# Performance work log

Measured on AMD Instinct MI355X. Metric: run time of the kernel, lower is better.

Reference implementation:

```python
import jax, jax.numpy as jnp
import numpy as np

D_MODEL = 1024
N_HEADS = 16
DFF = 4096
B, S = 2, 2048
EPS = 1e-6


def _dense_params(key, d_in, d_out):
    kw, kb = jax.random.split(key)
    w = jax.random.normal(kw, (d_in, d_out), jnp.float32) * 0.02
    b = jax.random.normal(kb, (d_out,), jnp.float32) * 0.02
    return w, b


def setup_inputs() -> dict:
    key = jax.random.key(0)
    ks = jax.random.split(key, 20)
    inp = {
        "x": jax.random.normal(ks[0], (B, S, D_MODEL), jnp.float32),
        "enc_output": jax.random.normal(ks[1], (B, S, D_MODEL), jnp.float32),
        # causal look-ahead mask: 1 where attention is NOT allowed
        "look_ahead_mask": jnp.triu(jnp.ones((S, S), jnp.float32), k=1)[None, None],
        "padding_mask": (jax.random.uniform(ks[2], (B, 1, 1, S)) < 0.1).astype(jnp.float32),
    }
    names = ["mha1_wq", "mha1_wk", "mha1_wv", "mha1_wo",
             "mha2_wq", "mha2_wk", "mha2_wv", "mha2_wo"]
    for i, n in enumerate(names):
        w, b = _dense_params(ks[3 + i], D_MODEL, D_MODEL)
        inp[n] = w
        inp[n.replace("w", "b")] = b
    inp["ffn_w1"], inp["ffn_b1"] = _dense_params(ks[11], D_MODEL, DFF)
    inp["ffn_w2"], inp["ffn_b2"] = _dense_params(ks[12], DFF, D_MODEL)
    for i, n in enumerate(["ln1", "ln2", "ln3"]):
        inp[n + "_g"] = jnp.ones((D_MODEL,), jnp.float32)
        inp[n + "_b"] = jnp.zeros((D_MODEL,), jnp.float32)
    return inp


def _layernorm(x, g, b):
    mu = jnp.mean(x, axis=-1, keepdims=True)
    var = jnp.mean(jnp.square(x - mu), axis=-1, keepdims=True)
    return (x - mu) * jax.lax.rsqrt(var + EPS) * g + b


def _mha(v, k, q, mask, wq, bq, wk, bk, wv, bv, wo, bo):
    Bq, Sq, D = q.shape
    depth = D // N_HEADS

    def split(t):  # [B,S,D] -> [B,H,S,depth]
        return t.reshape(t.shape[0], -1, N_HEADS, depth).transpose(0, 2, 1, 3)

    qh = split(q @ wq + bq)
    kh = split(k @ wk + bk)
    vh = split(v @ wv + bv)
    logits = jnp.einsum("bhqd,bhkd->bhqk", qh, kh) / jnp.sqrt(jnp.float32(depth))
    if mask is not None:
        logits = logits + mask * (-1e9)
    attn = jax.nn.softmax(logits, axis=-1)
    out = jnp.einsum("bhqk,bhkd->bhqd", attn, vh)
    out = out.transpose(0, 2, 1, 3).reshape(Bq, Sq, D)
    return out @ wo + bo


def reference(x, enc_output, look_ahead_mask, padding_mask,
              mha1_wq, mha1_bq, mha1_wk, mha1_bk, mha1_wv, mha1_bv, mha1_wo, mha1_bo,
              mha2_wq, mha2_bq, mha2_wk, mha2_bk, mha2_wv, mha2_bv, mha2_wo, mha2_bo,
              ffn_w1, ffn_b1, ffn_w2, ffn_b2,
              ln1_g, ln1_b, ln2_g, ln2_b, ln3_g, ln3_b):
    # self-attention (training=False -> dropout is identity)
    attn1 = _mha(x, x, x, look_ahead_mask,
                 mha1_wq, mha1_bq, mha1_wk, mha1_bk, mha1_wv, mha1_bv, mha1_wo, mha1_bo)
    out1 = _layernorm(x + attn1, ln1_g, ln1_b)
    # cross-attention: q from decoder, k/v from encoder output
    attn2 = _mha(enc_output, enc_output, out1, padding_mask,
                 mha2_wq, mha2_bq, mha2_wk, mha2_bk, mha2_wv, mha2_bv, mha2_wo, mha2_bo)
    out2 = _layernorm(out1 + attn2, ln2_g, ln2_b)
    ffn = jax.nn.relu(out2 @ ffn_w1 + ffn_b1) @ ffn_w2 + ffn_b2
    return _layernorm(out2 + ffn, ln3_g, ln3_b)
```

## Files before the change

kernel.cpp:

```cpp
#include <hip/hip_runtime.h>
#include <hip/hip_bf16.h>
#include <stdint.h>

#define DM   1024
#define NH   16
#define SS   2048
#define BB   2
#define MT   4096

typedef __attribute__((ext_vector_type(8))) short short8;
typedef __attribute__((ext_vector_type(4))) float f32x4;

typedef __attribute__((address_space(1))) const unsigned int as1_uint;
typedef __attribute__((address_space(3))) unsigned int as3_uint;

__device__ __forceinline__ void async16(const void* g, void* l) {
  __builtin_amdgcn_global_load_lds((as1_uint*)g, (as3_uint*)l, 16, 0, 0);
}

#define WAITV(n) asm volatile("s_waitcnt vmcnt(" #n ")" ::: "memory")
#define BARRIER_SB() do { __builtin_amdgcn_s_barrier(); __builtin_amdgcn_sched_barrier(0); } while (0)
#define EXP2(x) __builtin_amdgcn_exp2f(x)

__device__ __forceinline__ unsigned short f2bf(float f) {
  union { float f; unsigned u; } c; c.f = f;
  unsigned r = c.u + 0x7fffu + ((c.u >> 16) & 1u);
  return (unsigned short)(r >> 16);
}

__device__ __forceinline__ unsigned cvt_pk_bf16(float lo, float hi) {
  unsigned r;
  asm("v_cvt_pk_bf16_f32 %0, %1, %2" : "=v"(r) : "v"(lo), "v"(hi));
  return r;
}

__device__ __forceinline__ float swz16(float x) {
  return __uint_as_float((unsigned)__builtin_amdgcn_ds_swizzle((int)__float_as_uint(x), 0x401F));
}

__device__ __forceinline__ void xcd_swz(int& bx, int& by, int& bz) {
  int GX = gridDim.x, GY = gridDim.y;
  int nwg = GX * GY * gridDim.z;
  int old = blockIdx.x + GX * (blockIdx.y + GY * blockIdx.z);
  int f2 = (old & 7) * (nwg >> 3) + (old >> 3);
  bz = f2 / (GX * GY);
  int rem = f2 % (GX * GY);
  bx = rem / GY;
  by = rem % GY;
}

__global__ __launch_bounds__(256) void k_conv2(
    const float* __restrict__ a, const float* __restrict__ b,
    unsigned short* __restrict__ oa, unsigned short* __restrict__ ob) {
  int bxr = blockIdx.x;
  const float* in = (bxr < 4096) ? a : b;
  unsigned short* out = (bxr < 4096) ? oa : ob;
  int i = ((bxr & 4095) * 256 + threadIdx.x) * 4;
  float4 v = *(const float4*)(in + i);
  uint2 u;
  u.x = (unsigned)f2bf(v.x) | ((unsigned)f2bf(v.y) << 16);
  u.y = (unsigned)f2bf(v.z) | ((unsigned)f2bf(v.w) << 16);
  *(uint2*)(out + i) = u;
}

__global__ __launch_bounds__(256) void k_transpose_bf16(
    const float* __restrict__ in, unsigned short* __restrict__ out, int R, int C) {
  __shared__ float t[64][65];
  int c0 = blockIdx.x * 64, r0 = blockIdx.y * 64;
  int tx = threadIdx.x & 63, ty = threadIdx.x >> 6;
#pragma unroll
  for (int i = 0; i < 16; i++)
    t[ty + i * 4][tx] = in[(size_t)(r0 + ty + i * 4) * C + c0 + tx];
  __syncthreads();
#pragma unroll
  for (int i = 0; i < 16; i++)
    out[(size_t)(c0 + ty + i * 4) * R + r0 + tx] = f2bf(t[tx][ty + i * 4]);
}

struct PtrArr { const float* p[8]; };
__global__ __launch_bounds__(256) void k_transpose8(
    PtrArr ps, unsigned short* __restrict__ out0) {
  __shared__ float t[64][65];
  const float* in = ps.p[blockIdx.z];
  unsigned short* out = out0 + (size_t)blockIdx.z * 1048576;
  int c0 = blockIdx.x * 64, r0 = blockIdx.y * 64;
  int tx = threadIdx.x & 63, ty = threadIdx.x >> 6;
#pragma unroll
  for (int i = 0; i < 16; i++)
    t[ty + i * 4][tx] = in[(size_t)(r0 + ty + i * 4) * 1024 + c0 + tx];
  __syncthreads();
#pragma unroll
  for (int i = 0; i < 16; i++)
    out[(size_t)(c0 + ty + i * 4) * 1024 + r0 + tx] = f2bf(t[tx][ty + i * 4]);
}

template<int BM, int OUT_MODE, bool RELU, bool RESID, bool SPLITK>
__global__ __launch_bounds__(256) void k_gemm(
    const unsigned short* __restrict__ A,
    const unsigned short* __restrict__ Bt,
    const float* __restrict__ bias,
    const float* __restrict__ resid,
    void* __restrict__ outp, void* __restrict__ outp2,
    int M, int N, int K, int KS) {
  __shared__ unsigned short Alds[3][BM * 32];
  __shared__ unsigned short Blds[3][128 * 32];
  int tid = threadIdx.x;
  int w = tid >> 6, lane = tid & 63;
  int l15 = lane & 15, l4 = lane >> 4;
  int bxs, bys, bzs;
  xcd_swz(bxs, bys, bzs);
  int brow = bys * BM, bcol = bxs * 128;

  constexpr int MR = 4;
  constexpr int NR = (BM == 128) ? 4 : 2;
  int wr = (BM == 128) ? (w >> 1) : 0;
  int wc = (BM == 128) ? (w & 1) : w;
  int rbase = wr * 64;
  int cbase = wc * (NR * 16);

  f32x4 acc[MR][NR];
#pragma unroll
  for (int i = 0; i < MR; i++)
#pragma unroll
    for (int j = 0; j < NR; j++) acc[i][j] = (f32x4){0.f, 0.f, 0.f, 0.f};

#define STAGEG(bufi, kk) do {                                                  \
    _Pragma("unroll")                                                          \
    for (int c = 0; c < BM / 64; c++) {                                        \
      int elem = (c * 256 + tid) * 8;                                          \
      int row = elem >> 5, col = elem & 31;                                    \
      async16(A + (size_t)(brow + row) * K + (kk) + col, &Alds[bufi][elem]);   \
    }                                                                          \
    _Pragma("unroll")                                                          \
    for (int c = 0; c < 2; c++) {                                              \
      int elem = (c * 256 + tid) * 8;                                          \
      int row = elem >> 5, col = elem & 31;                                    \
      async16(Bt + (size_t)(bcol + row) * K + (kk) + col, &Blds[bufi][elem]);  \
    } } while (0)

  int kbeg = SPLITK ? bzs * KS : 0;
  int nk = KS / 32;
  STAGEG(0, kbeg);
  if (nk > 1) {
    STAGEG(1, kbeg + 32);
    if (BM == 128) WAITV(4); else WAITV(3);
  } else {
    WAITV(0);
  }
  BARRIER_SB();

  for (int t = 0; t < nk; t++) {
    int buf = t % 3;
    if (t + 2 < nk) STAGEG((t + 2) % 3, kbeg + (t + 2) * 32);
    short8 af[MR], bfr[NR];
#pragma unroll
    for (int i = 0; i < MR; i++)
      af[i] = *(const short8*)&Alds[buf][(rbase + i * 16 + l15) * 32 + l4 * 8];
#pragma unroll
    for (int j = 0; j < NR; j++)
      bfr[j] = *(const short8*)&Blds[buf][(cbase + j * 16 + l15) * 32 + l4 * 8];
#pragma unroll
    for (int i = 0; i < MR; i++)
#pragma unroll
      for (int j = 0; j < NR; j++)
        acc[i][j] = __builtin_amdgcn_mfma_f32_16x16x32_bf16(af[i], bfr[j], acc[i][j], 0, 0, 0);
    if (t + 2 < nk) {
      if (BM == 128) WAITV(4); else WAITV(3);
    } else if (t + 1 < nk) {
      WAITV(0);
    }
    if (t + 1 < nk) BARRIER_SB();
  }
#undef STAGEG

  void* op = (SPLITK && bzs) ? outp2 : outp;
#pragma unroll
  for (int i = 0; i < MR; i++)
#pragma unroll
    for (int j = 0; j < NR; j++) {
      int row = brow + rbase + i * 16 + l4 * 4;
      int col = bcol + cbase + j * 16 + l15;
      float bs = (SPLITK || !bias) ? 0.f : bias[col];
#pragma unroll
      for (int r = 0; r < 4; r++) {
        float v = acc[i][j][r] + bs;
        if (RESID) v += resid[(size_t)(row + r) * N + col];
        if (RELU) v = fmaxf(v, 0.f);
        if (OUT_MODE == 0) ((float*)op)[(size_t)(row + r) * N + col] = v;
        else               ((unsigned short*)op)[(size_t)(row + r) * N + col] = f2bf(v);
      }
    }
}

__global__ __launch_bounds__(256) void k_gemm_qkv(
    const unsigned short* __restrict__ a0, const unsigned short* __restrict__ a1,
    const unsigned short* __restrict__ a2,
    const unsigned short* __restrict__ Bt,
    const float* __restrict__ b0, const float* __restrict__ b1, const float* __restrict__ b2,
    unsigned short* __restrict__ o0, unsigned short* __restrict__ o1, unsigned short* __restrict__ o2,
    int vmat, int M, int K) {
  __shared__ unsigned short Alds[3][128 * 32];
  __shared__ unsigned short Blds[3][128 * 32];
  int tid = threadIdx.x;
  int w = tid >> 6, lane = tid & 63;
  int wr = w >> 1, wc = w & 1;
  int l15 = lane & 15, l4 = lane >> 4;
  int bxs, bys, z;
  xcd_swz(bxs, bys, z);
  const unsigned short* A  = (z == 0) ? a0 : (z == 1) ? a1 : a2;
  const unsigned short* Bz = Bt + (size_t)z * 1048576;
  int brow = bys * 128, bcol = bxs * 128;

  f32x4 acc[4][4];
#pragma unroll
  for (int i = 0; i < 4; i++)
#pragma unroll
    for (int j = 0; j < 4; j++) acc[i][j] = (f32x4){0.f, 0.f, 0.f, 0.f};

#define STAGEQ(bufi, kk) do {                                                  \
    _Pragma("unroll")                                                          \
    for (int c = 0; c < 2; c++) {                                              \
      int elem = (c * 256 + tid) * 8;                                          \
      int row = elem >> 5, col = elem & 31;                                    \
      async16(A + (size_t)(brow + row) * K + (kk) + col, &Alds[bufi][elem]);   \
      async16(Bz + (size_t)(bcol + row) * K + (kk) + col, &Blds[bufi][elem]);  \
    } } while (0)

  int nk = K / 32;
  STAGEQ(0, 0);
  STAGEQ(1, 32);
  WAITV(4);
  BARRIER_SB();

  for (int t = 0; t < nk; t++) {
    int buf = t % 3;
    if (t + 2 < nk) STAGEQ((t + 2) % 3, (t + 2) * 32);
    short8 af[4], bfr[4];
#pragma unroll
    for (int i = 0; i < 4; i++) {
      af[i]  = *(const short8*)&Alds[buf][(wr * 64 + i * 16 + l15) * 32 + l4 * 8];
      bfr[i] = *(const short8*)&Blds[buf][(wc * 64 + i * 16 + l15) * 32 + l4 * 8];
    }
#pragma unroll
    for (int i = 0; i < 4; i++)
#pragma unroll
      for (int j = 0; j < 4; j++)
        acc[i][j] = __builtin_amdgcn_mfma_f32_16x16x32_bf16(af[i], bfr[j], acc[i][j], 0, 0, 0);
    if (t + 2 < nk) WAITV(4);
    else if (t + 1 < nk) WAITV(0);
    if (t + 1 < nk) BARRIER_SB();
  }
#undef STAGEQ

  const float* bias = (z == 0) ? b0 : (z == 1) ? b1 : b2;
  unsigned short* op = (z == 0) ? o0 : (z == 1) ? o1 : o2;
  bool tr = (z == vmat);
#pragma unroll
  for (int i = 0; i < 4; i++)
#pragma unroll
    for (int j = 0; j < 4; j++) {
      int row = brow + wr * 64 + i * 16 + l4 * 4;
      int colL = bcol + wc * 64 + j * 16 + l15;
      float bs = bias[colL];
#pragma unroll
      for (int r = 0; r < 4; r++) {
        float v = acc[i][j][r] + bs;
        if (tr) op[(size_t)colL * M + row + r] = f2bf(v);
        else    op[(size_t)(row + r) * 1024 + colL] = f2bf(v);
      }
    }
}

template<bool CAUSAL, int NF>
__global__ __launch_bounds__(256) void k_attn(
    const unsigned short* __restrict__ Q,
    const unsigned short* __restrict__ Kb,
    const unsigned short* __restrict__ Vt,
    const float* __restrict__ pm,
    unsigned short* __restrict__ out) {
  __shared__ unsigned short Klds[3][64 * 64];
  __shared__ unsigned short Vlds[3][64 * 64];
  __shared__ unsigned short Pw[4][NF][16 * 72];
  int tid = threadIdx.x, w = tid >> 6, lane = tid & 63;
  int l15 = lane & 15, l4 = lane >> 4;
  int h = blockIdx.y, b = blockIdx.z;
  const float SC = 0.125f * 1.44269504089f;
  const int NPASS = CAUSAL ? 2 : 1;

#define STAGE(bufi, kt_) do {                                                  \
    _Pragma("unroll")                                                          \
    for (int c = 0; c < 2; c++) {                                              \
      int e0 = w * 1024 + c * 512;                                             \
      int elem = e0 + lane * 8;                                                \
      int row_ = elem >> 6;                                                    \
      int col_ = (elem & 63) ^ ((row_ & 7) << 3);                              \
      async16(Kb + (size_t)(b * SS + (kt_) * 64 + row_) * DM + h * 64 + col_,  \
              &Klds[bufi][elem]);                                              \
      async16(Vt + (size_t)(h * 64 + row_) * MT + b * SS + (kt_) * 64 + col_,  \
              &Vlds[bufi][elem]);                                              \
    } } while (0)

  for (int pass = 0; pass < NPASS; pass++) {
    int qt = CAUSAL ? (pass == 0 ? (31 - (int)blockIdx.x) : (int)blockIdx.x)
                    : (int)blockIdx.x;
    int qbase = qt * (NF * 64) + w * (NF * 16);

    short8 qf[NF][2];
#pragma unroll
    for (int f = 0; f < NF; f++) {
      size_t qrow = (size_t)b * SS + qbase + f * 16 + l15;
#pragma unroll
      for (int ks = 0; ks < 2; ks++)
        qf[f][ks] = *(const short8*)(Q + qrow * DM + h * 64 + ks * 32 + l4 * 8);
    }

    float mrow[NF], lrow[NF];
    f32x4 accO[NF][4];
#pragma unroll
    for (int f = 0; f < NF; f++) {
      mrow[f] = -1e30f; lrow[f] = 0.f;
#pragma unroll
      for (int d = 0; d < 4; d++) accO[f][d] = (f32x4){0.f, 0.f, 0.f, 0.f};
    }

    int ktend = CAUSAL ? qt : (SS / 64 - 1);
    if (pass) BARRIER_SB();
    STAGE(0, 0);
    if (ktend >= 1) { STAGE(1, 1); WAITV(4); } else { WAITV(0); }
    BARRIER_SB();

    for (int kt = 0; kt <= ktend; kt++) {
      int buf = kt % 3;
      if (kt + 2 <= ktend) STAGE((kt + 2) % 3, kt + 2);

      bool active = !CAUSAL || (kt * 64 <= qbase + NF * 16 - 1);
      if (active) {
        f32x4 sa[NF][4];
#pragma unroll
        for (int f = 0; f < NF; f++)
#pragma unroll
          for (int nt = 0; nt < 4; nt++) sa[f][nt] = (f32x4){0.f, 0.f, 0.f, 0.f};
        __builtin_amdgcn_s_setprio(1);
#pragma unroll
        for (int ks = 0; ks < 2; ks++)
#pragma unroll
          for (int nt = 0; nt < 4; nt++) {
            int kr = nt * 16 + l15;
            short8 kf = *(const short8*)&Klds[buf][kr * 64 + ((ks * 32 + l4 * 8) ^ ((kr & 7) << 3))];
#pragma unroll
            for (int f = 0; f < NF; f++)
              sa[f][nt] = __builtin_amdgcn_mfma_f32_16x16x32_bf16(kf, qf[f][ks], sa[f][nt], 0, 0, 0);
          }
        __builtin_amdgcn_s_setprio(0);

        float pmb[16];
        if (!CAUSAL) {
#pragma unroll
          for (int nt = 0; nt < 4; nt++) {
            float4 pmv = *(const float4*)(pm + b * SS + kt * 64 + nt * 16 + l4 * 4);
#pragma unroll
            for (int r = 0; r < 4; r++) pmb[nt * 4 + r] = ((const float*)&pmv)[r] * -1e30f;
          }
        }
        bool diag = CAUSAL && (kt * 64 + 63 > qbase);

        float sv[NF][16], tm[NF];
#pragma unroll
        for (int f = 0; f < NF; f++) {
          if (CAUSAL && !diag) {
#pragma unroll
            for (int i = 0; i < 16; i++) sv[f][i] = sa[f][i >> 2][i & 3] * SC;
          } else if (CAUSAL) {
#pragma unroll
            for (int nt = 0; nt < 4; nt++)
#pragma unroll
              for (int r = 0; r < 4; r++) {
                float s = sa[f][nt][r] * SC;
                int kg = kt * 64 + nt * 16 + l4 * 4 + r;
                int qg = qbase + f * 16 + l15;
                if (kg > qg) s = -1e30f;
                sv[f][nt * 4 + r] = s;
              }
          } else {
#pragma unroll
            for (int i = 0; i < 16; i++)
              sv[f][i] = fmaf(sa[f][i >> 2][i & 3], SC, pmb[i]);
          }
          float t8[8];
#pragma unroll
          for (int i = 0; i < 8; i++) t8[i] = fmaxf(sv[f][i], sv[f][i + 8]);
#pragma unroll
          for (int i = 0; i < 4; i++) t8[i] = fmaxf(t8[i], t8[i + 4]);
          t8[0] = fmaxf(t8[0], t8[1]);
          t8[2] = fmaxf(t8[2], t8[3]);
          tm[f] = fmaxf(t8[0], t8[2]);
        }

        float sA[NF];
#pragma unroll
        for (int f = 0; f < NF; f++) sA[f] = swz16(tm[f]);
#pragma unroll
        for (int f = 0; f < NF; f++) tm[f] = fmaxf(tm[f], sA[f]);
        float xA[NF];
#pragma unroll
        for (int f = 0; f < NF; f++) xA[f] = __shfl_xor(tm[f], 32);
#pragma unroll
        for (int f = 0; f < NF; f++) tm[f] = fmaxf(tm[f], xA[f]);

#pragma unroll
        for (int f = 0; f < NF; f++) {
          if (!__all(tm[f] - mrow[f] <= 8.f)) {
            float mnew = fmaxf(mrow[f], tm[f]);
            float corr = EXP2(mrow[f] - mnew);
            mrow[f] = mnew;
            lrow[f] *= corr;
#pragma unroll
            for (int r = 0; r < 4; r++) {
              float cq = __shfl(corr, l4 * 4 + r);
#pragma unroll
              for (int dt = 0; dt < 4; dt++) accO[f][dt][r] *= cq;
            }
          }

          float p[16];
#pragma unroll
          for (int i = 0; i < 16; i++) p[i] = EXP2(sv[f][i] - mrow[f]);
          float a8[8];
#pragma unroll
          for (int i = 0; i < 8; i++) a8[i] = p[i] + p[i + 8];
#pragma unroll
          for (int i = 0; i < 4; i++) a8[i] = a8[i] + a8[i + 4];
          lrow[f] += (a8[0] + a8[1]) + (a8[2] + a8[3]);

#pragma unroll
          for (int nt = 0; nt < 4; nt++) {
            uint2 u;
            u.x = cvt_pk_bf16(p[nt * 4 + 0], p[nt * 4 + 1]);
            u.y = cvt_pk_bf16(p[nt * 4 + 2], p[nt * 4 + 3]);
            *(uint2*)&Pw[w][f][l15 * 72 + nt * 16 + l4 * 4] = u;
          }
        }

        __builtin_amdgcn_s_setprio(1);
#pragma unroll
        for (int ks = 0; ks < 2; ks++) {
          short8 pf[NF];
#pragma unroll
          for (int f = 0; f < NF; f++)
            pf[f] = *(const short8*)&Pw[w][f][l15 * 72 + ks * 32 + l4 * 8];
#pragma unroll
          for (int dt = 0; dt < 4; dt++) {
            int vr = dt * 16 + l15;
            short8 vf = *(const short8*)&Vlds[buf][vr * 64 + ((ks * 32 + l4 * 8) ^ ((vr & 7) << 3))];
#pragma unroll
            for (int f = 0; f < NF; f++)
              accO[f][dt] = __builtin_amdgcn_mfma_f32_16x16x32_bf16(pf[f], vf, accO[f][dt], 0, 0, 0);
          }
        }
        __builtin_amdgcn_s_setprio(0);
      }

      if (kt + 2 <= ktend) WAITV(4);
      else if (kt + 1 <= ktend) WAITV(0);
      if (kt + 1 <= ktend) BARRIER_SB();
    }

#pragma unroll
    for (int f = 0; f < NF; f++) {
      lrow[f] += swz16(lrow[f]);
      lrow[f] += __shfl_xor(lrow[f], 32);
    }
#pragma unroll
    for (int f = 0; f < NF; f++)
#pragma unroll
      for (int r = 0; r < 4; r++) {
        float lq = __shfl(lrow[f], l4 * 4 + r);
        float inv = 1.f / lq;
        size_t row = (size_t)b * SS + qbase + f * 16 + l4 * 4 + r;
#pragma unroll
        for (int dt = 0; dt < 4; dt++)
          out[row * DM + h * 64 + dt * 16 + l15] = f2bf(accO[f][dt][r] * inv);
      }
  }
#undef STAGE
}

__global__ __launch_bounds__(256) void k_ln(
    const float* __restrict__ in, const float* __restrict__ in2,
    const float* __restrict__ resid, const float* __restrict__ bias,
    const float* __restrict__ g, const float* __restrict__ bb,
    float* __restrict__ outf, unsigned short* __restrict__ outb) {
  int row = blockIdx.x, tid = threadIdx.x;
  int w = tid >> 6;
  __shared__ float red[4];
  float4 v = *(const float4*)(in + (size_t)row * 1024 + tid * 4);
  if (in2) {
    float4 v2 = *(const float4*)(in2 + (size_t)row * 1024 + tid * 4);
    v.x += v2.x; v.y += v2.y; v.z += v2.z; v.w += v2.w;
  }
  if (resid) {
    float4 v2 = *(const float4*)(resid + (size_t)row * 1024 + tid * 4);
    v.x += v2.x; v.y += v2.y; v.z += v2.z; v.w += v2.w;
  }
  if (bias) {
    float4 v2 = *(const float4*)(bias + tid * 4);
    v.x += v2.x; v.y += v2.y; v.z += v2.z; v.w += v2.w;
  }
  float s = v.x + v.y + v.z + v.w;
#pragma unroll
  for (int d = 1; d < 64; d <<= 1) s += __shfl_xor(s, d);
  if ((tid & 63) == 0) red[w] = s;
  __syncthreads();
  float mu = (red[0] + red[1] + red[2] + red[3]) * (1.f / 1024.f);
  float d0 = v.x - mu, d1 = v.y - mu, d2 = v.z - mu, d3 = v.w - mu;
  float q = d0 * d0 + d1 * d1 + d2 * d2 + d3 * d3;
#pragma unroll
  for (int d = 1; d < 64; d <<= 1) q += __shfl_xor(q, d);
  __syncthreads();
  if ((tid & 63) == 0) red[w] = q;
  __syncthreads();
  float var = (red[0] + red[1] + red[2] + red[3]) * (1.f / 1024.f);
  float rs = rsqrtf(var + 1e-6f);
  float4 gg = *(const float4*)(g + tid * 4);
  float4 bv = *(const float4*)(bb + tid * 4);
  float y0 = d0 * rs * gg.x + bv.x;
  float y1 = d1 * rs * gg.y + bv.y;
  float y2 = d2 * rs * gg.z + bv.z;
  float y3 = d3 * rs * gg.w + bv.w;
  if (outf) {
    float4 o; o.x = y0; o.y = y1; o.z = y2; o.w = y3;
    *(float4*)(outf + (size_t)row * 1024 + tid * 4) = o;
  }
  if (outb) {
    uint2 u;
    u.x = (unsigned)f2bf(y0) | ((unsigned)f2bf(y1) << 16);
    u.y = (unsigned)f2bf(y2) | ((unsigned)f2bf(y3) << 16);
    *(uint2*)(outb + (size_t)row * 1024 + tid * 4) = u;
  }
}

extern "C" void kernel_launch(void* const* d_in, const int* in_sizes, int n_in,
                              void* d_out, int out_size, void* d_ws, size_t ws_size,
                              hipStream_t stream) {
  const float* x    = (const float*)d_in[0];
  const float* enc  = (const float*)d_in[1];
  const float* pm   = (const float*)d_in[3];
  const float* wq1  = (const float*)d_in[4];   const float* bq1 = (const float*)d_in[5];
  const float* wk1  = (const float*)d_in[6];   const float* bk1 = (const float*)d_in[7];
  const float* wv1  = (const float*)d_in[8];   const float* bv1 = (const float*)d_in[9];
  const float* wo1  = (const float*)d_in[10];  const float* bo1 = (const float*)d_in[11];
  const float* wq2  = (const float*)d_in[12];  const float* bq2 = (const float*)d_in[13];
  const float* wk2  = (const float*)d_in[14];  const float* bk2 = (const float*)d_in[15];
  const float* wv2  = (const float*)d_in[16];  const float* bv2 = (const float*)d_in[17];
  const float* wo2  = (const float*)d_in[18];  const float* bo2 = (const float*)d_in[19];
  const float* fw1  = (const float*)d_in[20];  const float* fb1 = (const float*)d_in[21];
  const float* fw2  = (const float*)d_in[22];  const float* fb2 = (const float*)d_in[23];
  const float* ln1g = (const float*)d_in[24];  const float* ln1b = (const float*)d_in[25];
  const float* ln2g = (const float*)d_in[26];  const float* ln2b = (const float*)d_in[27];
  const float* ln3g = (const float*)d_in[28];  const float* ln3b = (const float*)d_in[29];

  char* ws = (char*)d_ws;
  unsigned short* XB = (unsigned short*)(ws + 0);
  unsigned short* EB = (unsigned short*)(ws + 8388608);
  unsigned short* Qb = (unsigned short*)(ws + 16777216);
  unsigned short* Kb = (unsigned short*)(ws + 25165824);
  unsigned short* Vt = (unsigned short*)(ws + 33554432);
  unsigned short* AT = (unsigned short*)(ws + 41943040);
  float*          T  = (float*)(ws + 50331648);
  float*          R  = (float*)(ws + 67108864);
  unsigned short* RB = (unsigned short*)(ws + 83886080);
  unsigned short* WT0 = (unsigned short*)(ws + 92274688);
  unsigned short* W1T = (unsigned short*)(ws + 92274688 + 16777216);
  unsigned short* W2T = (unsigned short*)(ws + 92274688 + 25165824);
  unsigned short* H   = (unsigned short*)(ws + 0);
  float*          T1  = (float*)(ws + 33554432);
  float*          T1o = (float*)(ws + 16777216);

  k_conv2<<<8192, 256, 0, stream>>>(x, enc, XB, EB);
  PtrArr ptrs;
  ptrs.p[0] = wq1; ptrs.p[1] = wk1; ptrs.p[2] = wv1; ptrs.p[3] = wo1;
  ptrs.p[4] = wq2; ptrs.p[5] = wk2; ptrs.p[6] = wv2; ptrs.p[7] = wo2;
  k_transpose8<<<dim3(16, 16, 8), 256, 0, stream>>>(ptrs, WT0);
  k_transpose_bf16<<<dim3(64, 16), 256, 0, stream>>>(fw1, W1T, 1024, 4096);
  k_transpose_bf16<<<dim3(16, 64), 256, 0, stream>>>(fw2, W2T, 4096, 1024);

  k_gemm_qkv<<<dim3(8, 32, 3), 256, 0, stream>>>(XB, XB, XB, WT0, bq1, bk1, bv1,
                                                 Qb, Kb, Vt, 2, MT, DM);
  k_attn<true, 1><<<dim3(16, 16, 2), 256, 0, stream>>>(Qb, Kb, Vt, nullptr, AT);
  k_gemm<64, 0, false, false, true><<<dim3(8, 64, 2), 256, 0, stream>>>(
      AT, WT0 + 3 * 1048576, nullptr, nullptr, T, T1o, MT, DM, DM, 512);
  k_ln<<<4096, 256, 0, stream>>>(T, T1o, x, bo1, ln1g, ln1b, R, RB);

  k_gemm_qkv<<<dim3(8, 32, 3), 256, 0, stream>>>(RB, EB, EB, WT0 + 4 * 1048576,
                                                 bq2, bk2, bv2, Qb, Kb, Vt, 2, MT, DM);
  k_attn<false, 2><<<dim3(16, 16, 2), 256, 0, stream>>>(Qb, Kb, Vt, pm, AT);
  k_gemm<64, 0, false, false, true><<<dim3(8, 64, 2), 256, 0, stream>>>(
      AT, WT0 + 7 * 1048576, nullptr, nullptr, T, T1o, MT, DM, DM, 512);
  k_ln<<<4096, 256, 0, stream>>>(T, T1o, R, bo2, ln2g, ln2b, R, RB);

  k_gemm<128, 1, true, false, false><<<dim3(32, 32), 256, 0, stream>>>(
      RB, W1T, fb1, nullptr, H, nullptr, MT, 4096, DM, 1024);
  k_gemm<64, 0, false, false, true><<<dim3(8, 64, 2), 256, 0, stream>>>(
      H, W2T, nullptr, nullptr, T, T1, MT, DM, 4096, 2048);
  k_ln<<<4096, 256, 0, stream>>>(T, T1, R, fb2, ln3g, ln3b, (float*)d_out, nullptr);
}
```

Before: 452.9 us.

## Use 256x256-tile 512-thread GEMM with 4-way split-K for FFN layers

Adds a new GEMM kernel with 256x256 output tiles, 8 waves, and double-buffered 64-wide K stages held in 128KB of dynamic LDS. Loads for the next stage are interleaved between quarter-tile MFMA clusters. Both FFN matmuls now use this kernel. The second one uses a 4-way split-K whose partial sums are added inside a layernorm kernel that now takes four inputs. The goal is more data reuse per block and a single wave of 256 blocks over the CUs. In exchange, each CU holds only one block because of the LDS size, and split-K writes more fp32 partial data.

```diff
diff --git a/kernel.cpp b/kernel.cpp
--- a/kernel.cpp
+++ b/kernel.cpp
@@ -92,6 +92,159 @@
 #pragma unroll
   for (int i = 0; i < 16; i++)
     out[(size_t)(c0 + ty + i * 4) * 1024 + r0 + tx] = f2bf(t[tx][ty + i * 4]);
+}
+
+__device__ __forceinline__ void stage_half(
+    unsigned short* lds, int dst_off, const unsigned short* __restrict__ src,
+    int sbase, int c0, int K, int kk, int tid) {
+#pragma unroll
+  for (int c = 0; c < 2; c++) {
+    int e = ((c0 + c) * 512 + tid) * 8;
+    int r_ = e >> 6, s_ = e & 63;
+    async16(src + (size_t)(sbase + r_) * K + kk + (s_ ^ ((r_ & 4) << 2)),
+            &lds[dst_off + e]);
+  }
+}
+
+__device__ __forceinline__ void read_afrags(
+    const unsigned short* lds, int aoff, int wm, int rh, int l15, int l4,
+    short8 af[4][2]) {
+#pragma unroll
+  for (int i = 0; i < 4; i++) {
+    int arow = wm * 128 + rh * 64 + i * 16 + l15;
+#pragma unroll
+    for (int ks = 0; ks < 2; ks++)
+      af[i][ks] = *(const short8*)&lds[aoff + arow * 64 +
+          ((ks * 32 + l4 * 8) ^ ((arow & 4) << 2))];
+  }
+}
+
+__device__ __forceinline__ void read_bfrags(
+    const unsigned short* lds, int boff, int wn, int ch, int l15, int l4,
+    short8 bf[2][2]) {
+#pragma unroll
+  for (int j = 0; j < 2; j++) {
+    int brw = wn * 64 + ch * 32 + j * 16 + l15;
+#pragma unroll
+    for (int ks = 0; ks < 2; ks++)
+      bf[j][ks] = *(const short8*)&lds[boff + brw * 64 +
+          ((ks * 32 + l4 * 8) ^ ((brw & 4) << 2))];
+  }
+}
+
+#define MFMA_CL(RH, CH)                                                        \
+  __builtin_amdgcn_s_barrier();                                                \
+  asm volatile("s_waitcnt lgkmcnt(0)" ::: "memory");                           \
+  __builtin_amdgcn_sched_barrier(0);                                           \
+  __builtin_amdgcn_s_setprio(1);                                               \
+  _Pragma("unroll")                                                            \
+  for (int ks = 0; ks < 2; ks++)                                               \
+    _Pragma("unroll")                                                          \
+    for (int i = 0; i < 4; i++)                                                \
+      _Pragma("unroll")                                                        \
+      for (int j = 0; j < 2; j++)                                              \
+        acc[(RH) * 4 + i][(CH) * 2 + j] =                                      \
+            __builtin_amdgcn_mfma_f32_16x16x32_bf16(                           \
+                af[i][ks], bf[j][ks], acc[(RH) * 4 + i][(CH) * 2 + j], 0, 0, 0); \
+  __builtin_amdgcn_s_setprio(0);
+
+template<int OUT_MODE, bool RELU>
+__global__ __launch_bounds__(512, 2) void k_gemm256(
+    const unsigned short* __restrict__ A,
+    const unsigned short* __restrict__ Bt,
+    const float* __restrict__ bias,
+    void* __restrict__ p0, void* __restrict__ p1,
+    void* __restrict__ p2, void* __restrict__ p3,
+    int M, int N, int K, int KS) {
+  extern __shared__ unsigned short lds[];
+  int tid = threadIdx.x;
+  int wid = tid >> 6, lane = tid & 63;
+  int wm = wid >> 2, wn = wid & 3;
+  int l15 = lane & 15, l4 = lane >> 4;
+  int brow = blockIdx.y * 256, bcol = blockIdx.x * 256;
+  int bz = blockIdx.z;
+  int kbeg = bz * KS;
+  int nk = KS / 64;
+
+  f32x4 acc[8][4];
+#pragma unroll
+  for (int i = 0; i < 8; i++)
+#pragma unroll
+    for (int j = 0; j < 4; j++) acc[i][j] = (f32x4){0.f, 0.f, 0.f, 0.f};
+
+  short8 af[4][2], bf[2][2];
+
+  stage_half(lds, 32768, Bt, bcol, 0, K, kbeg, tid);
+  stage_half(lds, 32768, Bt, bcol, 2, K, kbeg, tid);
+  stage_half(lds, 0,     A,  brow, 0, K, kbeg, tid);
+  stage_half(lds, 0,     A,  brow, 2, K, kbeg, tid);
+  WAITV(0);
+  __builtin_amdgcn_s_barrier();
+
+  for (int t = 0; t < nk; t++) {
+    int buf = t & 1, nb = buf ^ 1;
+    int aoff = buf * 16384, boff = 32768 + buf * 16384;
+    int naoff = nb * 16384, nboff = 32768 + nb * 16384;
+    int kk2 = kbeg + (t + 1) * 64;
+    bool more = (t + 1 < nk);
+
+    read_afrags(lds, aoff, wm, 0, l15, l4, af);
+    read_bfrags(lds, boff, wn, 0, l15, l4, bf);
+    if (more) {
+      stage_half(lds, nboff, Bt, bcol, 0, K, kk2, tid);
+      stage_half(lds, nboff, Bt, bcol, 2, K, kk2, tid);
+    }
+    MFMA_CL(0, 0);
+    __builtin_amdgcn_s_barrier();
+
+    read_bfrags(lds, boff, wn, 1, l15, l4, bf);
+    if (more) stage_half(lds, naoff, A, brow, 0, K, kk2, tid);
+    MFMA_CL(0, 1);
+    __builtin_amdgcn_s_barrier();
+
+    read_afrags(lds, aoff, wm, 1, l15, l4, af);
+    read_bfrags(lds, boff, wn, 0, l15, l4, bf);
+    if (more) stage_half(lds, naoff, A, brow, 2, K, kk2, tid);
+    MFMA_CL(1, 0);
+    __builtin_amdgcn_s_barrier();
+
+    read_bfrags(lds, boff, wn, 1, l15, l4, bf);
+    MFMA_CL(1, 1);
+    if (more) {
+      WAITV(0);
+      __builtin_amdgcn_s_barrier();
+    }
+  }
+
+  if (OUT_MODE == 1) {
+    unsigned short* op = (unsigned short*)p0;
+#pragma unroll
+    for (int ai = 0; ai < 8; ai++)
+#pragma unroll
+      for (int bj = 0; bj < 4; bj++) {
+        int row = brow + wm * 128 + ai * 16 + l4 * 4;
+        int col = bcol + wn * 64 + bj * 16 + l15;
+        float bs = bias[col];
+#pragma unroll
+        for (int r = 0; r < 4; r++) {
+          float v = acc[ai][bj][r] + bs;
+          if (RELU) v = fmaxf(v, 0.f);
+          op[(size_t)(row + r) * N + col] = f2bf(v);
+        }
+      }
+  } else {
+    float* op = (float*)((bz == 0) ? p0 : (bz == 1) ? p1 : (bz == 2) ? p2 : p3);
+#pragma unroll
+    for (int ai = 0; ai < 8; ai++)
+#pragma unroll
+      for (int bj = 0; bj < 4; bj++) {
+        int row = brow + wm * 128 + ai * 16 + l4 * 4;
+        int col = bcol + wn * 64 + bj * 16 + l15;
+#pragma unroll
+        for (int r = 0; r < 4; r++)
+          op[(size_t)(row + r) * N + col] = acc[ai][bj][r];
+      }
+  }
 }
 
 template<int BM, int OUT_MODE, bool RELU, bool RESID, bool SPLITK>
@@ -487,6 +640,7 @@
 
 __global__ __launch_bounds__(256) void k_ln(
     const float* __restrict__ in, const float* __restrict__ in2,
+    const float* __restrict__ in3, const float* __restrict__ in4,
     const float* __restrict__ resid, const float* __restrict__ bias,
     const float* __restrict__ g, const float* __restrict__ bb,
     float* __restrict__ outf, unsigned short* __restrict__ outb) {
@@ -496,6 +650,14 @@
   float4 v = *(const float4*)(in + (size_t)row * 1024 + tid * 4);
   if (in2) {
     float4 v2 = *(const float4*)(in2 + (size_t)row * 1024 + tid * 4);
+    v.x += v2.x; v.y += v2.y; v.z += v2.z; v.w += v2.w;
+  }
+  if (in3) {
+    float4 v2 = *(const float4*)(in3 + (size_t)row * 1024 + tid * 4);
+    v.x += v2.x; v.y += v2.y; v.z += v2.z; v.w += v2.w;
+  }
+  if (in4) {
+    float4 v2 = *(const float4*)(in4 + (size_t)row * 1024 + tid * 4);
     v.x += v2.x; v.y += v2.y; v.z += v2.z; v.w += v2.w;
   }
   if (resid) {
@@ -575,6 +737,10 @@
   unsigned short* H   = (unsigned short*)(ws + 0);
   float*          T1  = (float*)(ws + 33554432);
   float*          T1o = (float*)(ws + 16777216);
+  float*          P0  = T;
+  float*          P1  = (float*)(ws + 33554432);
+  float*          P2  = (float*)(ws + 83886080);
+  float*          P3  = (float*)(ws + 100663296);
 
   k_conv2<<<8192, 256, 0, stream>>>(x, enc, XB, EB);
   PtrArr ptrs;
@@ -589,18 +755,34 @@
   k_attn<true, 1><<<dim3(16, 16, 2), 256, 0, stream>>>(Qb, Kb, Vt, nullptr, AT);
   k_gemm<64, 0, false, false, true><<<dim3(8, 64, 2), 256, 0, stream>>>(
       AT, WT0 + 3 * 1048576, nullptr, nullptr, T, T1o, MT, DM, DM, 512);
-  k_ln<<<4096, 256, 0, stream>>>(T, T1o, x, bo1, ln1g, ln1b, R, RB);
+  k_ln<<<4096, 256, 0, stream>>>(T, T1o, nullptr, nullptr, x, bo1, ln1g, ln1b, R, RB);
 
   k_gemm_qkv<<<dim3(8, 32, 3), 256, 0, stream>>>(RB, EB, EB, WT0 + 4 * 1048576,
                                                  bq2, bk2, bv2, Qb, Kb, Vt, 2, MT, DM);
   k_attn<false, 2><<<dim3(16, 16, 2), 256, 0, stream>>>(Qb, Kb, Vt, pm, AT);
   k_gemm<64, 0, false, false, true><<<dim3(8, 64, 2), 256, 0, stream>>>(
       AT, WT0 + 7 * 1048576, nullptr, nullptr, T, T1o, MT, DM, DM, 512);
-  k_ln<<<4096, 256, 0, stream>>>(T, T1o, R, bo2, ln2g, ln2b, R, RB);
-
-  k_gemm<128, 1, true, false, false><<<dim3(32, 32), 256, 0, stream>>>(
-      RB, W1T, fb1, nullptr, H, nullptr, MT, 4096, DM, 1024);
-  k_gemm<64, 0, false, false, true><<<dim3(8, 64, 2), 256, 0, stream>>>(
-      H, W2T, nullptr, nullptr, T, T1, MT, DM, 4096, 2048);
-  k_ln<<<4096, 256, 0, stream>>>(T, T1, R, fb2, ln3g, ln3b, (float*)d_out, nullptr);
-}
+  k_ln<<<4096, 256, 0, stream>>>(T, T1o, nullptr, nullptr, R, bo2, ln2g, ln2b, R, RB);
+
+  hipError_t ea = hipFuncSetAttribute(
+      reinterpret_cast<const void*>(k_gemm256<1, true>),
+      hipFuncAttributeMaxDynamicSharedMemorySize, 131072);
+  hipError_t eb = hipFuncSetAttribute(
+      reinterpret_cast<const void*>(k_gemm256<0, false>),
+      hipFuncAttributeMaxDynamicSharedMemorySize, 131072);
+  if (ea == hipSuccess && eb == hipSuccess) {
+    k_gemm256<1, true><<<dim3(16, 16, 1), 512, 131072, stream>>>(
+        RB, W1T, fb1, H, nullptr, nullptr, nullptr, MT, 4096, DM, DM);
+    k_gemm256<0, false><<<dim3(4, 16, 4), 512, 131072, stream>>>(
+        H, W2T, nullptr, P0, P1, P2, P3, MT, DM, 4096, 1024);
+    k_ln<<<4096, 256, 0, stream>>>(P0, P1, P2, P3, R, fb2, ln3g, ln3b,
+                                   (float*)d_out, nullptr);
+  } else {
+    k_gemm<128, 1, true, false, false><<<dim3(32, 32), 256, 0, stream>>>(
+        RB, W1T, fb1, nullptr, H, nullptr, MT, 4096, DM, 1024);
+    k_gemm<64, 0, false, false, true><<<dim3(8, 64, 2), 256, 0, stream>>>(
+        H, W2T, nullptr, nullptr, T, T1, MT, DM, 4096, 2048);
+    k_ln<<<4096, 256, 0, stream>>>(T, T1, nullptr, nullptr, R, fb2, ln3g, ln3b,
+                                   (float*)d_out, nullptr);
+  }
+}
```

After: 431.1 us. 4.8% less time.
